# Performance work log

Measured on AMD Instinct MI355X. Metric: run time of the kernel, lower is better.

The kernel has to match this reference:

```python
import jax, jax.numpy as jnp
import numpy as np

EPS = 1e-6
TAU = 0.07


def setup_inputs() -> dict:
    key = jax.random.key(0)
    kx, ky = jax.random.split(key)
    B, D = 4096, 1024
    x = jax.random.normal(kx, (B, D), dtype=jnp.float32)
    y = jax.random.normal(ky, (B, D), dtype=jnp.float32)
    return {"x": x, "y": y}


def reference(x, y):
    B = x.shape[0]
    # torch CosineSimilarity: dot / (max(||x||, eps) * max(||y||, eps))
    xn = x / jnp.maximum(jnp.linalg.norm(x, axis=-1, keepdims=True), EPS)
    yn = y / jnp.maximum(jnp.linalg.norm(y, axis=-1, keepdims=True), EPS)
    S = jnp.einsum('id,jd->ij', xn, yn)          # [B, B] cosine sims, S[i,j]=cos(x_i,y_j)
    E = jnp.exp(S / TAU)                          # bounded: |S|<=1 so exp <= e^{1/0.07}
    diag = jnp.diagonal(E)
    # original: sum_j (exp + eps) + eps  ->  sum_j exp + B*eps + eps
    extra = B * EPS + EPS
    row_denom = jnp.sum(E, axis=1) + extra        # x->y direction (loop 1)
    col_denom = jnp.sum(E, axis=0) + extra        # y->x direction (loop 2)
    coef = -1.0 / (2.0 * B)
    loss = coef * (jnp.sum(jnp.log(diag / row_denom)) + jnp.sum(jnp.log(diag / col_denom)))
    return loss
```

## Files before the change

kernel.cpp:

```cpp
#include <hip/hip_runtime.h>

#define NB 4096
#define DK 1024
#define EPSF 1e-6f
#define QS 32.0f

typedef __attribute__((ext_vector_type(8))) int   i32x8_t;
typedef __attribute__((ext_vector_type(4))) int   i32x4_t;
typedef __attribute__((ext_vector_type(4))) float f32x4_t;

#if defined(__has_builtin)
#if __has_builtin(__builtin_amdgcn_cvt_scalef32_pk_fp4_f32)
#define HW_FP4 1
#endif
#endif


__device__ __forceinline__ unsigned enc4(float v) {
    const float a = fabsf(v);
    unsigned c = (a >= 0.25f) + (a >= 0.75f) + (a >= 1.25f) + (a >= 1.75f)
               + (a >= 2.5f)  + (a >= 3.5f)  + (a >= 5.0f);
    return c | ((v < 0.f) ? 8u : 0u);
}

__global__ __launch_bounds__(256) void normalize_rows(
    const float* __restrict__ x, const float* __restrict__ y,
    unsigned char* __restrict__ xq, unsigned char* __restrict__ yq,
    float* __restrict__ sdiag, float* __restrict__ zerobuf)
{
    const int t = threadIdx.x;
    const int gid = blockIdx.x * 256 + t;
    if (gid < 2 * NB) zerobuf[gid] = 0.f;

    const int wave = t >> 6;
    const int lane = t & 63;
    const int row  = blockIdx.x * 4 + wave;

    const float4* xr = reinterpret_cast<const float4*>(x + (size_t)row * DK);
    const float4* yr = reinterpret_cast<const float4*>(y + (size_t)row * DK);

    float4 xv[4], yv[4];
    float ssx = 0.f, ssy = 0.f, sxy = 0.f;
    #pragma unroll
    for (int jj = 0; jj < 4; ++jj) {
        xv[jj] = xr[lane * 4 + jj];
        yv[jj] = yr[lane * 4 + jj];
        ssx += xv[jj].x*xv[jj].x + xv[jj].y*xv[jj].y + xv[jj].z*xv[jj].z + xv[jj].w*xv[jj].w;
        ssy += yv[jj].x*yv[jj].x + yv[jj].y*yv[jj].y + yv[jj].z*yv[jj].z + yv[jj].w*yv[jj].w;
        sxy += xv[jj].x*yv[jj].x + xv[jj].y*yv[jj].y + xv[jj].z*yv[jj].z + xv[jj].w*yv[jj].w;
    }
    #pragma unroll
    for (int off = 1; off < 64; off <<= 1) {
        ssx += __shfl_xor(ssx, off, 64);
        ssy += __shfl_xor(ssy, off, 64);
        sxy += __shfl_xor(sxy, off, 64);
    }
    const float invx = 1.0f / fmaxf(sqrtf(ssx), EPSF);
    const float invy = 1.0f / fmaxf(sqrtf(ssy), EPSF);
    const float sx = invx * QS;
    const float sy = invy * QS;

    float fx[16], fy[16];
    #pragma unroll
    for (int jj = 0; jj < 4; ++jj) {
        fx[jj*4+0] = xv[jj].x; fx[jj*4+1] = xv[jj].y;
        fx[jj*4+2] = xv[jj].z; fx[jj*4+3] = xv[jj].w;
        fy[jj*4+0] = yv[jj].x; fy[jj*4+1] = yv[jj].y;
        fy[jj*4+2] = yv[jj].z; fy[jj*4+3] = yv[jj].w;
    }

    unsigned xb0, xb1, yb0, yb1;
#ifdef HW_FP4
    #define CVT8(dst, f, s)                                                        \
        dst = __builtin_amdgcn_cvt_scalef32_pk_fp4_f32(0u,  (f)[0]*(s), (f)[1]*(s), 1.0f, 0); \
        dst = __builtin_amdgcn_cvt_scalef32_pk_fp4_f32(dst, (f)[2]*(s), (f)[3]*(s), 1.0f, 1); \
        dst = __builtin_amdgcn_cvt_scalef32_pk_fp4_f32(dst, (f)[4]*(s), (f)[5]*(s), 1.0f, 2); \
        dst = __builtin_amdgcn_cvt_scalef32_pk_fp4_f32(dst, (f)[6]*(s), (f)[7]*(s), 1.0f, 3)
    CVT8(xb0, fx,     sx);
    CVT8(xb1, fx + 8, sx);
    CVT8(yb0, fy,     sy);
    CVT8(yb1, fy + 8, sy);
    #undef CVT8
#else
    unsigned xb[2] = {0u, 0u}, yb[2] = {0u, 0u};
    #pragma unroll
    for (int j = 0; j < 16; ++j) {
        xb[j >> 3] |= enc4(fx[j] * sx) << ((j & 7) * 4);
        yb[j >> 3] |= enc4(fy[j] * sy) << ((j & 7) * 4);
    }
    xb0 = xb[0]; xb1 = xb[1]; yb0 = yb[0]; yb1 = yb[1];
#endif

    const int p = row >> 4, r = row & 15;
    const unsigned off = (unsigned)p * 8192 + (lane >> 3) * 1024 + r * 64
                       + (lane & 7) * 8;
    *reinterpret_cast<uint2*>(xq + off) = make_uint2(xb0, xb1);
    *reinterpret_cast<uint2*>(yq + off) = make_uint2(yb0, yb1);

    if (lane == 0) sdiag[row] = sxy * invx * invy;
}

__global__ __launch_bounds__(512, 2) void gemm_exp_sums(
    const unsigned char* __restrict__ xq, const unsigned char* __restrict__ yq,
    float* __restrict__ rowsum, float* __restrict__ colsum)
{
    const int t    = threadIdx.x;
    const int lane = t & 63;
    const int wave = t >> 6;
    const int q    = lane >> 4;
    const int l15  = lane & 15;

    const int R0 = blockIdx.y * 128;
    const int C0 = blockIdx.x * 256;
    const int wRow = (wave >> 2) * 64;
    const int wCol = (wave & 3) * 64;

    f32x4_t acc[4][4];
    #pragma unroll
    for (int i = 0; i < 4; i++)
        #pragma unroll
        for (int j = 0; j < 4; j++)
            acc[i][j] = (f32x4_t){0.f, 0.f, 0.f, 0.f};

    const unsigned char* pA = xq + (size_t)((R0 + wRow) >> 4) * 8192 + l15 * 64 + q * 16;
    const unsigned char* pB = yq + (size_t)((C0 + wCol) >> 4) * 8192 + l15 * 64 + q * 16;

    #pragma unroll
    for (int kb = 0; kb < 8; ++kb) {
        i32x4_t a4[4], b4[4];
        #pragma unroll
        for (int i = 0; i < 4; ++i) {
            a4[i] = *reinterpret_cast<const i32x4_t*>(pA + (size_t)i * 8192 + kb * 1024);
            b4[i] = *reinterpret_cast<const i32x4_t*>(pB + (size_t)i * 8192 + kb * 1024);
        }
        #pragma unroll
        for (int mt = 0; mt < 4; ++mt) {
            const i32x8_t af = {a4[mt][0], a4[mt][1], a4[mt][2], a4[mt][3], 0, 0, 0, 0};
            #pragma unroll
            for (int nt = 0; nt < 4; ++nt) {
                const i32x8_t bf = {b4[nt][0], b4[nt][1], b4[nt][2], b4[nt][3], 0, 0, 0, 0};
                acc[mt][nt] = __builtin_amdgcn_mfma_scale_f32_16x16x128_f8f6f4(
                    af, bf, acc[mt][nt],
                    4, 4,
                    0, 0x7F7F7F7F,
                    0, 0x7F7F7F7F);
            }
        }
    }

    const float kScale = (float)(1.0 / (1024.0 * 0.07 * 0.6931471805599453));
    float csum[4] = {0.f, 0.f, 0.f, 0.f};
    #pragma unroll
    for (int mt = 0; mt < 4; ++mt) {
        float rsum[4] = {0.f, 0.f, 0.f, 0.f};
        #pragma unroll
        for (int nt = 0; nt < 4; ++nt) {
            #pragma unroll
            for (int r = 0; r < 4; ++r) {
                const float e = exp2f(acc[mt][nt][r] * kScale);
                rsum[r]  += e;
                csum[nt] += e;
            }
        }
        #pragma unroll
        for (int r = 0; r < 4; ++r) {
            float v = rsum[r];
            v += __shfl_xor(v, 1, 64);
            v += __shfl_xor(v, 2, 64);
            v += __shfl_xor(v, 4, 64);
            v += __shfl_xor(v, 8, 64);
            if (l15 == 0)
                atomicAdd(&rowsum[R0 + wRow + mt * 16 + q * 4 + r], v);
        }
    }
    #pragma unroll
    for (int nt = 0; nt < 4; ++nt) {
        float v = csum[nt];
        v += __shfl_xor(v, 16, 64);
        v += __shfl_xor(v, 32, 64);
        if (lane < 16)
            atomicAdd(&colsum[C0 + wCol + nt * 16 + l15], v);
    }
}

__global__ __launch_bounds__(1024) void finalize(
    const float* __restrict__ rowsum, const float* __restrict__ colsum,
    const float* __restrict__ sdiag, float* __restrict__ out)
{
    const float extra = (float)(NB * 1e-6 + 1e-6);
    double local = 0.0;
    for (int i = threadIdx.x; i < NB; i += 1024) {
        local += (double)sdiag[i] * (2.0 / 0.07)
               - (double)logf(rowsum[i] + extra)
               - (double)logf(colsum[i] + extra);
    }
    #pragma unroll
    for (int off = 1; off < 64; off <<= 1)
        local += __shfl_xor(local, off, 64);
    __shared__ double dred[16];
    const int wave = threadIdx.x >> 6;
    if ((threadIdx.x & 63) == 0) dred[wave] = local;
    __syncthreads();
    if (threadIdx.x == 0) {
        double tot = 0.0;
        #pragma unroll
        for (int w = 0; w < 16; ++w) tot += dred[w];
        out[0] = (float)(tot * (-1.0 / (2.0 * NB)));
    }
}

extern "C" void kernel_launch(void* const* d_in, const int* in_sizes, int n_in,
                              void* d_out, int out_size, void* d_ws, size_t ws_size,
                              hipStream_t stream)
{
    const float* x = (const float*)d_in[0];
    const float* y = (const float*)d_in[1];
    float* out = (float*)d_out;

    char* ws = (char*)d_ws;
    unsigned char* xq = (unsigned char*)ws;
    unsigned char* yq = (unsigned char*)(ws + (size_t)2 * 1024 * 1024);
    float* rowsum = (float*)(ws + (size_t)8 * 1024 * 1024);
    float* colsum = rowsum + NB;
    float* sdiag  = colsum + NB;

    normalize_rows<<<NB / 4, 256, 0, stream>>>(x, y, xq, yq, sdiag, rowsum);

    dim3 grid(16, 32);
    gemm_exp_sums<<<grid, 512, 0, stream>>>(xq, yq, rowsum, colsum);

    finalize<<<1, 1024, 0, stream>>>(rowsum, colsum, sdiag, out);
}
```

Measured before the change: 116.9 us.

## Stage FP4 GEMM tiles through double-buffered LDS with async global-to-LDS loads

The GEMM kernel now copies A and B tiles into LDS with global_load_lds, double-buffered across the K loop, so the next K block loads while MFMAs run on the current one. The quantized layout written by normalize_rows is XOR-swizzled to avoid LDS bank conflicts. Block tiles shrink to 128x128 with 256 threads and a doubled grid. This aims to hide global load latency and share tiles between waves, at the cost of per-step barriers and more atomics from the larger grid.

```diff
diff --git a/kernel.cpp b/kernel.cpp
--- a/kernel.cpp
+++ b/kernel.cpp
@@ -15,6 +15,12 @@
 #endif
 #endif
 
+
+__device__ __forceinline__ void async16(const void* g, void* lds) {
+    __builtin_amdgcn_global_load_lds(
+        (const __attribute__((address_space(1))) void*)g,
+        (__attribute__((address_space(3))) void*)lds, 16, 0, 0);
+}
 
 __device__ __forceinline__ unsigned enc4(float v) {
     const float a = fabsf(v);
@@ -93,17 +99,19 @@
 
     const int p = row >> 4, r = row & 15;
     const unsigned off = (unsigned)p * 8192 + (lane >> 3) * 1024 + r * 64
-                       + (lane & 7) * 8;
+                       + ((((lane & 7) >> 1) ^ (r & 3)) << 4) + (lane & 1) * 8;
     *reinterpret_cast<uint2*>(xq + off) = make_uint2(xb0, xb1);
     *reinterpret_cast<uint2*>(yq + off) = make_uint2(yb0, yb1);
 
     if (lane == 0) sdiag[row] = sxy * invx * invy;
 }
 
-__global__ __launch_bounds__(512, 2) void gemm_exp_sums(
+__global__ __launch_bounds__(256, 4) void gemm_exp_sums(
     const unsigned char* __restrict__ xq, const unsigned char* __restrict__ yq,
     float* __restrict__ rowsum, float* __restrict__ colsum)
 {
+    __shared__ __align__(16) unsigned char LDS[2][16384];
+
     const int t    = threadIdx.x;
     const int lane = t & 63;
     const int wave = t >> 6;
@@ -111,9 +119,9 @@
     const int l15  = lane & 15;
 
     const int R0 = blockIdx.y * 128;
-    const int C0 = blockIdx.x * 256;
-    const int wRow = (wave >> 2) * 64;
-    const int wCol = (wave & 3) * 64;
+    const int C0 = blockIdx.x * 128;
+    const int wRow = (wave >> 1) * 64;
+    const int wCol = (wave & 1) * 64;
 
     f32x4_t acc[4][4];
     #pragma unroll
@@ -122,29 +130,54 @@
         for (int j = 0; j < 4; j++)
             acc[i][j] = (f32x4_t){0.f, 0.f, 0.f, 0.f};
 
-    const unsigned char* pA = xq + (size_t)((R0 + wRow) >> 4) * 8192 + l15 * 64 + q * 16;
-    const unsigned char* pB = yq + (size_t)((C0 + wCol) >> 4) * 8192 + l15 * 64 + q * 16;
-
-    #pragma unroll
+    const unsigned char* srcA =
+        xq + (size_t)((R0 >> 4) + 2 * wave) * 8192 + lane * 16;
+    const unsigned char* srcB =
+        yq + (size_t)((C0 >> 4) + 2 * wave) * 8192 + lane * 16;
+
+    auto issue = [&](int kb, int buf) {
+        #pragma unroll
+        for (int pp = 0; pp < 2; ++pp) {
+            async16(srcA + pp * 8192 + kb * 1024,
+                    &LDS[buf][(2 * wave + pp) * 1024]);
+            async16(srcB + pp * 8192 + kb * 1024,
+                    &LDS[buf][8192 + (2 * wave + pp) * 1024]);
+        }
+    };
+
+    issue(0, 0);
+
+    const int sl = (q ^ (l15 & 3)) << 4;
+
+    #pragma unroll 1
     for (int kb = 0; kb < 8; ++kb) {
-        i32x4_t a4[4], b4[4];
-        #pragma unroll
-        for (int i = 0; i < 4; ++i) {
-            a4[i] = *reinterpret_cast<const i32x4_t*>(pA + (size_t)i * 8192 + kb * 1024);
-            b4[i] = *reinterpret_cast<const i32x4_t*>(pB + (size_t)i * 8192 + kb * 1024);
+        const int buf = kb & 1;
+        __builtin_amdgcn_s_waitcnt(0xF70);
+        __syncthreads();
+        if (kb < 7) issue(kb + 1, buf ^ 1);
+
+        i32x8_t bfr[4];
+        #pragma unroll
+        for (int nt = 0; nt < 4; ++nt) {
+            const i32x4_t v = *reinterpret_cast<const i32x4_t*>(
+                &LDS[buf][8192 + ((wCol >> 4) + nt) * 1024 + l15 * 64 + sl]);
+            bfr[nt][0] = v[0]; bfr[nt][1] = v[1]; bfr[nt][2] = v[2]; bfr[nt][3] = v[3];
+            bfr[nt][4] = 0;    bfr[nt][5] = 0;    bfr[nt][6] = 0;    bfr[nt][7] = 0;
         }
         #pragma unroll
         for (int mt = 0; mt < 4; ++mt) {
-            const i32x8_t af = {a4[mt][0], a4[mt][1], a4[mt][2], a4[mt][3], 0, 0, 0, 0};
+            const i32x4_t v = *reinterpret_cast<const i32x4_t*>(
+                &LDS[buf][((wRow >> 4) + mt) * 1024 + l15 * 64 + sl]);
+            i32x8_t af;
+            af[0] = v[0]; af[1] = v[1]; af[2] = v[2]; af[3] = v[3];
+            af[4] = 0;    af[5] = 0;    af[6] = 0;    af[7] = 0;
             #pragma unroll
-            for (int nt = 0; nt < 4; ++nt) {
-                const i32x8_t bf = {b4[nt][0], b4[nt][1], b4[nt][2], b4[nt][3], 0, 0, 0, 0};
+            for (int nt = 0; nt < 4; ++nt)
                 acc[mt][nt] = __builtin_amdgcn_mfma_scale_f32_16x16x128_f8f6f4(
-                    af, bf, acc[mt][nt],
+                    af, bfr[nt], acc[mt][nt],
                     4, 4,
                     0, 0x7F7F7F7F,
                     0, 0x7F7F7F7F);
-            }
         }
     }
 
@@ -226,8 +259,8 @@
 
     normalize_rows<<<NB / 4, 256, 0, stream>>>(x, y, xq, yq, sdiag, rowsum);
 
-    dim3 grid(16, 32);
-    gemm_exp_sums<<<grid, 512, 0, stream>>>(xq, yq, rowsum, colsum);
+    dim3 grid(32, 32);
+    gemm_exp_sums<<<grid, 256, 0, stream>>>(xq, yq, rowsum, colsum);
 
     finalize<<<1, 1024, 0, stream>>>(rowsum, colsum, sdiag, out);
 }
```

After: 95.59 us. 1.22x faster.
